# Kernel tuning notes

Hardware: AMD Instinct MI355X
Metric: run time of the kernel (lower is better)

The kernel has to match this reference:

```python
import jax, jax.numpy as jnp
import numpy as np

NUM_HEADS = 12


def setup_inputs() -> dict:
    key = jax.random.key(0)
    k1, k2, k3, k4, k5 = jax.random.split(key, 5)
    B, H, W, C = 8, 32, 32, 768
    x = jax.random.normal(k1, (B, H, W, C), dtype=jnp.float32)
    # torch nn.Linear weights: (out_features, in_features)
    qkv_w = jax.random.normal(k2, (3 * C, C), dtype=jnp.float32) * (C ** -0.5)
    qkv_b = jax.random.normal(k3, (3 * C,), dtype=jnp.float32) * 0.02
    proj_w = jax.random.normal(k4, (C, C), dtype=jnp.float32) * (C ** -0.5)
    proj_b = jax.random.normal(k5, (C,), dtype=jnp.float32) * 0.02
    return {"x": x, "qkv_w": qkv_w, "qkv_b": qkv_b, "proj_w": proj_w, "proj_b": proj_b}


def reference(x, qkv_w, qkv_b, proj_w, proj_b):
    B, H, W, C = x.shape
    nh = NUM_HEADS
    hd = C // nh
    scale = hd ** -0.5
    L = H * W
    # qkv projection: (B, L, 3C)
    qkv = jnp.einsum('bhwc,oc->bhwo', x, qkv_w) + qkv_b
    # -> (3, B*nh, L, hd)
    qkv = qkv.reshape(B, L, 3, nh, hd).transpose(2, 0, 3, 1, 4).reshape(3, B * nh, L, hd)
    q, k, v = qkv[0], qkv[1], qkv[2]
    # attention scores (B*nh, L, L)
    attn = jnp.einsum('bqd,bkd->bqk', q * scale, k)
    attn = jax.nn.softmax(attn, axis=-1)
    out = jnp.einsum('bqk,bkd->bqd', attn, v)  # (B*nh, L, hd)
    out = out.reshape(B, nh, H, W, hd).transpose(0, 2, 3, 1, 4).reshape(B, H, W, C)
    out = jnp.einsum('bhwc,oc->bhwo', out, proj_w) + proj_b
    return out
```

## Files before the change

kernel.cpp:

```cpp
#include <hip/hip_runtime.h>


typedef __attribute__((ext_vector_type(8))) __bf16 bf16x8;
typedef __attribute__((ext_vector_type(4))) __bf16 bf16x4;
typedef __attribute__((ext_vector_type(4))) float f32x4;

#define GLL16(g, l) __builtin_amdgcn_global_load_lds( \
    (const __attribute__((address_space(1))) void*)(g), \
    (__attribute__((address_space(3))) void*)(l), 16, 0, 0)

static __device__ __forceinline__ f32x4 mfma16(bf16x8 a, bf16x8 b, f32x4 c) {
  return __builtin_amdgcn_mfma_f32_16x16x32_bf16(a, b, c, 0, 0, 0);
}

static __device__ __forceinline__ float exp2_hw(float x) {
  return __builtin_amdgcn_exp2f(x);
}

static __device__ __forceinline__ int swz64(int row, int col) {
  return (row * 64 + col) ^ ((row & 7) << 3);
}

__global__ __launch_bounds__(256) void cvt_all(const float* __restrict__ x,
                                               const float* __restrict__ wq,
                                               const float* __restrict__ wp,
                                               __bf16* __restrict__ dst,
                                               int nx4, int nwq4, int total4) {
  const int i = blockIdx.x * 256 + threadIdx.x;
  if (i >= total4) return;
  const float* src;
  int off;
  if (i < nx4) { src = x; off = i; }
  else if (i < nx4 + nwq4) { src = wq; off = i - nx4; }
  else { src = wp; off = i - nx4 - nwq4; }
  const float4 v = *(const float4*)&src[(size_t)off * 4];
  bf16x4 o;
  o[0] = (__bf16)v.x; o[1] = (__bf16)v.y; o[2] = (__bf16)v.z; o[3] = (__bf16)v.w;
  *(bf16x4*)&dst[(size_t)i * 4] = o;
}

template <int EPI>
__global__ __launch_bounds__(256) void gemm_nt(const __bf16* __restrict__ A,
                                               const __bf16* __restrict__ Bw,
                                               const float* __restrict__ bias,
                                               float* __restrict__ out,
                                               __bf16* __restrict__ Qb,
                                               __bf16* __restrict__ Kb,
                                               __bf16* __restrict__ Vtb,
                                               int M, int N, int K) {
  __shared__ alignas(16) __bf16 smem[3 * 4096 * 2];
  const int tid = threadIdx.x;
  const int lane = tid & 63;
  const int wave = tid >> 6;
  const int wr = wave >> 1, wc = wave & 1;
  const int l15 = lane & 15, lhi = lane >> 4;
  const int mbase = blockIdx.x * 128;
  const int nbase = blockIdx.y * 128;

  f32x4 acc[4][4];
#pragma unroll
  for (int m = 0; m < 4; ++m)
#pragma unroll
    for (int n = 0; n < 4; ++n) acc[m][n] = (f32x4){0.f, 0.f, 0.f, 0.f};

  const int e0 = wave * 512 + lane * 8;
  const int e1 = e0 + 2048;
  const int ar0 = mbase + (e0 >> 5), ac0 = e0 & 31;
  const int ar1 = mbase + (e1 >> 5), ac1 = e1 & 31;
  const int br0 = nbase + (e0 >> 5);
  const int br1 = nbase + (e1 >> 5);

  const int nkt = K >> 5;

#define STAGE(t, bf) do { \
    const int kb_ = (t) << 5; \
    GLL16(A + (size_t)ar0 * K + kb_ + ac0, &smem[(bf) * 4096 + e0]); \
    GLL16(A + (size_t)ar1 * K + kb_ + ac1, &smem[(bf) * 4096 + e1]); \
    GLL16(Bw + (size_t)br0 * K + kb_ + ac0, &smem[12288 + (bf) * 4096 + e0]); \
    GLL16(Bw + (size_t)br1 * K + kb_ + ac1, &smem[12288 + (bf) * 4096 + e1]); \
  } while (0)

  STAGE(0, 0);
  STAGE(1, 1);

  int cur = 0, nx2 = 2;
  for (int kt = 0; kt < nkt; ++kt) {
    if (kt + 1 < nkt)
      asm volatile("s_waitcnt vmcnt(4)" ::: "memory");
    else
      asm volatile("s_waitcnt vmcnt(0)" ::: "memory");
    __builtin_amdgcn_s_barrier();
    asm volatile("" ::: "memory");
    if (kt + 2 < nkt) STAGE(kt + 2, nx2);

    const __bf16* bufA = &smem[cur * 4096];
    const __bf16* bufB = &smem[12288 + cur * 4096];
    bf16x8 a[4], b[4];
#pragma unroll
    for (int m = 0; m < 4; ++m)
      a[m] = *(const bf16x8*)&bufA[(wr * 64 + m * 16 + l15) * 32 + lhi * 8];
#pragma unroll
    for (int n = 0; n < 4; ++n)
      b[n] = *(const bf16x8*)&bufB[(wc * 64 + n * 16 + l15) * 32 + lhi * 8];
#pragma unroll
    for (int m = 0; m < 4; ++m)
#pragma unroll
      for (int n = 0; n < 4; ++n)
        acc[m][n] = mfma16(a[m], b[n], acc[m][n]);

    cur = (cur == 2) ? 0 : cur + 1;
    nx2 = (nx2 == 2) ? 0 : nx2 + 1;
  }
#undef STAGE

  if (EPI == 0 && nbase >= 1536) {
    __syncthreads();
    __bf16* ldsT = &smem[0];
#pragma unroll
    for (int n = 0; n < 4; ++n) {
      const int gl = wc * 64 + n * 16 + l15;
      const float bv = bias[nbase + gl];
#pragma unroll
      for (int m = 0; m < 4; ++m) {
        bf16x4 pk;
#pragma unroll
        for (int i = 0; i < 4; ++i) pk[i] = (__bf16)(acc[m][n][i] + bv);
        *(bf16x4*)&ldsT[gl * 136 + wr * 64 + m * 16 + lhi * 4] = pk;
      }
    }
    __syncthreads();
    const int r = tid >> 1;
    const int half = tid & 1;
    const int head = ((nbase - 1536) >> 6) + (r >> 6);
    const int d = r & 63;
    const int bb = mbase >> 10;
    const int lbase = mbase & 1023;
    __bf16* dst = Vtb + ((size_t)(bb * 12 + head) * 64 + d) * 1024 + lbase + half * 64;
    const __bf16* srcl = &ldsT[r * 136 + half * 64];
#pragma unroll
    for (int j = 0; j < 8; ++j)
      *(bf16x8*)&dst[j * 8] = *(const bf16x8*)&srcl[j * 8];
    return;
  }

#pragma unroll
  for (int n = 0; n < 4; ++n) {
    const int gcol = nbase + wc * 64 + n * 16 + l15;
    const float bv = bias[gcol];
    if (EPI == 1) {
#pragma unroll
      for (int m = 0; m < 4; ++m)
#pragma unroll
        for (int i = 0; i < 4; ++i) {
          const int grow = mbase + wr * 64 + m * 16 + lhi * 4 + i;
          out[(size_t)grow * N + gcol] = acc[m][n][i] + bv;
        }
    } else {
      const int three = gcol / 768;
      const int rem = gcol - three * 768;
      const int head = rem >> 6;
      const int d = rem & 63;
#pragma unroll
      for (int m = 0; m < 4; ++m)
#pragma unroll
        for (int i = 0; i < 4; ++i) {
          const int grow = mbase + wr * 64 + m * 16 + lhi * 4 + i;
          const int bb = grow >> 10;
          const int lrow = grow & 1023;
          const int bh = bb * 12 + head;
          const float v = acc[m][n][i] + bv;
          if (three == 0)
            Qb[((size_t)bh * 1024 + lrow) * 64 + d] = (__bf16)(v * 0.18033688f);
          else
            Kb[((size_t)bh * 1024 + lrow) * 64 + d] = (__bf16)v;
        }
    }
  }
}

__global__ __launch_bounds__(256) void attn_fwd(const __bf16* __restrict__ Q,
                                                const __bf16* __restrict__ Kg,
                                                const __bf16* __restrict__ Vt,
                                                __bf16* __restrict__ O) {
  __shared__ alignas(16) __bf16 lK[2][64 * 64];
  __shared__ alignas(16) __bf16 lV[2][64 * 64];
  __shared__ alignas(16) __bf16 lP[4][32 * 72];
  const int tid = threadIdx.x, lane = tid & 63, wave = tid >> 6;
  const int l15 = lane & 15, lhi = lane >> 4;
  const int bh = blockIdx.x, qt = blockIdx.y;
  const int b = bh / 12, head = bh % 12;

  bf16x8 q[2][2];
#pragma unroll
  for (int qn = 0; qn < 2; ++qn) {
    const int qrow = qt * 128 + wave * 32 + qn * 16 + l15;
#pragma unroll
    for (int kk = 0; kk < 2; ++kk)
      q[qn][kk] = *(const bf16x8*)&Q[((size_t)bh * 1024 + qrow) * 64 + kk * 32 + lhi * 8];
  }

  f32x4 o[2][4];
  float mrun[2], lrun[2];
#pragma unroll
  for (int m = 0; m < 2; ++m) {
#pragma unroll
    for (int n = 0; n < 4; ++n) o[m][n] = (f32x4){0.f, 0.f, 0.f, 0.f};
    mrun[m] = -3.0e38f; lrun[m] = 0.f;
  }

  const int q0b = wave * 1024 + lane * 16;
  const int q1b = q0b + 4096;
  const int p0b = q0b ^ (((q0b >> 7) & 7) << 4);
  const int p1b = q1b ^ (((q1b >> 7) & 7) << 4);
  const int e0 = q0b >> 1, e1 = q1b >> 1;
  const int kofs0 = p0b >> 1, kofs1 = p1b >> 1;
  const int vofs0 = (p0b >> 7) * 1024 + ((p0b & 127) >> 1);
  const int vofs1 = (p1b >> 7) * 1024 + ((p1b & 127) >> 1);

  const __bf16* kbase = Kg + (size_t)bh * 1024 * 64;
  const __bf16* vbase = Vt + (size_t)bh * 64 * 1024;

  GLL16(kbase + kofs0, &lK[0][e0]);
  GLL16(kbase + kofs1, &lK[0][e1]);
  GLL16(vbase + vofs0, &lV[0][e0]);
  GLL16(vbase + vofs1, &lV[0][e1]);
  __syncthreads();

  for (int kv = 0; kv < 16; ++kv) {
    const int cur = kv & 1;
    if (kv + 1 < 16) {
      const __bf16* knext = kbase + (kv + 1) * 4096;
      const int vadd = (kv + 1) * 64;
      GLL16(knext + kofs0, &lK[cur ^ 1][e0]);
      GLL16(knext + kofs1, &lK[cur ^ 1][e1]);
      GLL16(vbase + vadd + vofs0, &lV[cur ^ 1][e0]);
      GLL16(vbase + vadd + vofs1, &lV[cur ^ 1][e1]);
    }

    f32x4 s[4][2];
#pragma unroll
    for (int km = 0; km < 4; ++km) {
      bf16x8 k0 = *(const bf16x8*)&lK[cur][swz64(km * 16 + l15, lhi * 8)];
      bf16x8 k1 = *(const bf16x8*)&lK[cur][swz64(km * 16 + l15, 32 + lhi * 8)];
#pragma unroll
      for (int qn = 0; qn < 2; ++qn) {
        f32x4 z = (f32x4){0.f, 0.f, 0.f, 0.f};
        z = mfma16(k0, q[qn][0], z);
        z = mfma16(k1, q[qn][1], z);
        s[km][qn] = z;
      }
    }

    float lm[2];
#pragma unroll
    for (int qn = 0; qn < 2; ++qn) {
      float r = s[0][qn][0];
#pragma unroll
      for (int km = 0; km < 4; ++km)
#pragma unroll
        for (int i = 0; i < 4; ++i) r = fmaxf(r, s[km][qn][i]);
      lm[qn] = r;
    }

    const bool ok = (lm[0] - mrun[0] <= 8.f) && (lm[1] - mrun[1] <= 8.f);
    if (!__all(ok)) {
      float alpha[2];
#pragma unroll
      for (int qn = 0; qn < 2; ++qn) {
        float r = lm[qn];
        r = fmaxf(r, __shfl_xor(r, 16));
        r = fmaxf(r, __shfl_xor(r, 32));
        const float mnew = fmaxf(mrun[qn], r);
        alpha[qn] = exp2_hw(mrun[qn] - mnew);
        mrun[qn] = mnew;
        lrun[qn] *= alpha[qn];
      }
      float am[2][4];
#pragma unroll
      for (int m = 0; m < 2; ++m)
#pragma unroll
        for (int i = 0; i < 4; ++i) am[m][i] = __shfl(alpha[m], (lhi << 2) | i, 64);
#pragma unroll
      for (int m = 0; m < 2; ++m)
#pragma unroll
        for (int n = 0; n < 4; ++n)
#pragma unroll
          for (int i = 0; i < 4; ++i) o[m][n][i] *= am[m][i];
    }

#pragma unroll
    for (int qn = 0; qn < 2; ++qn) {
      float ps = 0.f;
#pragma unroll
      for (int km = 0; km < 4; ++km) {
        bf16x4 pk;
#pragma unroll
        for (int i = 0; i < 4; ++i) {
          const float p = exp2_hw(s[km][qn][i] - mrun[qn]);
          ps += p;
          pk[i] = (__bf16)p;
        }
        *(bf16x4*)&lP[wave][(qn * 16 + l15) * 72 + km * 16 + lhi * 4] = pk;
      }
      lrun[qn] += ps;
    }

    bf16x8 vf[4][2];
#pragma unroll
    for (int n = 0; n < 4; ++n)
#pragma unroll
      for (int kk = 0; kk < 2; ++kk)
        vf[n][kk] = *(const bf16x8*)&lV[cur][swz64(n * 16 + l15, kk * 32 + lhi * 8)];
#pragma unroll
    for (int m = 0; m < 2; ++m) {
      bf16x8 p0 = *(const bf16x8*)&lP[wave][(m * 16 + l15) * 72 + lhi * 8];
      bf16x8 p1 = *(const bf16x8*)&lP[wave][(m * 16 + l15) * 72 + 32 + lhi * 8];
#pragma unroll
      for (int n = 0; n < 4; ++n) {
        o[m][n] = mfma16(p0, vf[n][0], o[m][n]);
        o[m][n] = mfma16(p1, vf[n][1], o[m][n]);
      }
    }
    __syncthreads();
  }

  float inv2[2];
#pragma unroll
  for (int qn = 0; qn < 2; ++qn) {
    float r = lrun[qn];
    r += __shfl_xor(r, 16);
    r += __shfl_xor(r, 32);
    inv2[qn] = 1.f / r;
  }
  float im[2][4];
#pragma unroll
  for (int m = 0; m < 2; ++m)
#pragma unroll
    for (int i = 0; i < 4; ++i) im[m][i] = __shfl(inv2[m], (lhi << 2) | i, 64);
#pragma unroll
  for (int m = 0; m < 2; ++m)
#pragma unroll
    for (int i = 0; i < 4; ++i) {
      const int lrow = qt * 128 + wave * 32 + m * 16 + lhi * 4 + i;
#pragma unroll
      for (int n = 0; n < 4; ++n) {
        const int col = head * 64 + n * 16 + l15;
        O[((size_t)b * 1024 + lrow) * 768 + col] = (__bf16)(o[m][n][i] * im[m][i]);
      }
    }
}

extern "C" void kernel_launch(void* const* d_in, const int* in_sizes, int n_in,
                              void* d_out, int out_size, void* d_ws, size_t ws_size,
                              hipStream_t stream) {
  const float* x = (const float*)d_in[0];
  const float* qkv_w = (const float*)d_in[1];
  const float* qkv_b = (const float*)d_in[2];
  const float* proj_w = (const float*)d_in[3];
  const float* proj_b = (const float*)d_in[4];
  float* out = (float*)d_out;

  const size_t NX = (size_t)8192 * 768;
  const size_t NWQ = (size_t)2304 * 768;
  const size_t NWP = (size_t)768 * 768;
  const size_t SZ = (size_t)96 * 1024 * 64;

  __bf16* xb = (__bf16*)d_ws;
  __bf16* wqkvb = xb + NX;
  __bf16* wprojb = wqkvb + NWQ;
  __bf16* Q = wprojb + NWP;
  __bf16* K = Q + SZ;
  __bf16* Vt = K + SZ;
  __bf16* AO = Vt + SZ;

  const int nx4 = (int)(NX / 4), nwq4 = (int)(NWQ / 4), nwp4 = (int)(NWP / 4);
  const int total4 = nx4 + nwq4 + nwp4;
  cvt_all<<<(total4 + 255) / 256, 256, 0, stream>>>(x, qkv_w, proj_w, xb, nx4, nwq4, total4);

  gemm_nt<0><<<dim3(64, 18), 256, 0, stream>>>(xb, wqkvb, qkv_b, nullptr, Q, K, Vt,
                                               8192, 2304, 768);
  attn_fwd<<<dim3(96, 8), 256, 0, stream>>>(Q, K, Vt, AO);
  gemm_nt<1><<<dim3(64, 6), 256, 0, stream>>>(AO, wprojb, proj_b, out,
                                              nullptr, nullptr, nullptr, 8192, 768, 768);
}
```

Measured before the change: 123.5 us.

## Split attention block into 8 waves of 16 query rows each

The attention kernel now runs 512 threads (8 waves), each handling 16 query rows instead of 32. This halves per-wave register state and the K/V load work per thread, while K/V tiles in LDS are shared by twice as many waves. The goal is more waves in flight to hide latency. The cost is that each wave now reads the K and V fragments from LDS for only one 16-row MFMA tile instead of two, so LDS traffic per FLOP doubles, and barrier sync now spans 8 waves.

```diff
diff --git a/kernel.cpp b/kernel.cpp
--- a/kernel.cpp
+++ b/kernel.cpp
@@ -178,131 +178,99 @@
   }
 }
 
-__global__ __launch_bounds__(256) void attn_fwd(const __bf16* __restrict__ Q,
-                                                const __bf16* __restrict__ Kg,
-                                                const __bf16* __restrict__ Vt,
-                                                __bf16* __restrict__ O) {
+__global__ __launch_bounds__(512, 6) void attn_fwd(const __bf16* __restrict__ Q,
+                                                   const __bf16* __restrict__ Kg,
+                                                   const __bf16* __restrict__ Vt,
+                                                   __bf16* __restrict__ O) {
   __shared__ alignas(16) __bf16 lK[2][64 * 64];
   __shared__ alignas(16) __bf16 lV[2][64 * 64];
-  __shared__ alignas(16) __bf16 lP[4][32 * 72];
+  __shared__ alignas(16) __bf16 lP[8][16 * 72];
   const int tid = threadIdx.x, lane = tid & 63, wave = tid >> 6;
   const int l15 = lane & 15, lhi = lane >> 4;
   const int bh = blockIdx.x, qt = blockIdx.y;
   const int b = bh / 12, head = bh % 12;
 
-  bf16x8 q[2][2];
-#pragma unroll
-  for (int qn = 0; qn < 2; ++qn) {
-    const int qrow = qt * 128 + wave * 32 + qn * 16 + l15;
+  bf16x8 q[2];
+  {
+    const int qrow = qt * 128 + wave * 16 + l15;
 #pragma unroll
     for (int kk = 0; kk < 2; ++kk)
-      q[qn][kk] = *(const bf16x8*)&Q[((size_t)bh * 1024 + qrow) * 64 + kk * 32 + lhi * 8];
-  }
-
-  f32x4 o[2][4];
-  float mrun[2], lrun[2];
-#pragma unroll
-  for (int m = 0; m < 2; ++m) {
-#pragma unroll
-    for (int n = 0; n < 4; ++n) o[m][n] = (f32x4){0.f, 0.f, 0.f, 0.f};
-    mrun[m] = -3.0e38f; lrun[m] = 0.f;
-  }
-
-  const int q0b = wave * 1024 + lane * 16;
-  const int q1b = q0b + 4096;
+      q[kk] = *(const bf16x8*)&Q[((size_t)bh * 1024 + qrow) * 64 + kk * 32 + lhi * 8];
+  }
+
+  f32x4 o[4];
+  float mrun = -3.0e38f, lrun = 0.f;
+#pragma unroll
+  for (int n = 0; n < 4; ++n) o[n] = (f32x4){0.f, 0.f, 0.f, 0.f};
+
+  const int q0b = tid * 16;
   const int p0b = q0b ^ (((q0b >> 7) & 7) << 4);
-  const int p1b = q1b ^ (((q1b >> 7) & 7) << 4);
-  const int e0 = q0b >> 1, e1 = q1b >> 1;
-  const int kofs0 = p0b >> 1, kofs1 = p1b >> 1;
+  const int e0 = q0b >> 1;
+  const int kofs0 = p0b >> 1;
   const int vofs0 = (p0b >> 7) * 1024 + ((p0b & 127) >> 1);
-  const int vofs1 = (p1b >> 7) * 1024 + ((p1b & 127) >> 1);
 
   const __bf16* kbase = Kg + (size_t)bh * 1024 * 64;
   const __bf16* vbase = Vt + (size_t)bh * 64 * 1024;
 
   GLL16(kbase + kofs0, &lK[0][e0]);
-  GLL16(kbase + kofs1, &lK[0][e1]);
   GLL16(vbase + vofs0, &lV[0][e0]);
-  GLL16(vbase + vofs1, &lV[0][e1]);
   __syncthreads();
 
   for (int kv = 0; kv < 16; ++kv) {
     const int cur = kv & 1;
     if (kv + 1 < 16) {
-      const __bf16* knext = kbase + (kv + 1) * 4096;
-      const int vadd = (kv + 1) * 64;
-      GLL16(knext + kofs0, &lK[cur ^ 1][e0]);
-      GLL16(knext + kofs1, &lK[cur ^ 1][e1]);
-      GLL16(vbase + vadd + vofs0, &lV[cur ^ 1][e0]);
-      GLL16(vbase + vadd + vofs1, &lV[cur ^ 1][e1]);
-    }
-
-    f32x4 s[4][2];
+      GLL16(kbase + (kv + 1) * 4096 + kofs0, &lK[cur ^ 1][e0]);
+      GLL16(vbase + (kv + 1) * 64 + vofs0, &lV[cur ^ 1][e0]);
+    }
+
+    f32x4 s[4];
 #pragma unroll
     for (int km = 0; km < 4; ++km) {
       bf16x8 k0 = *(const bf16x8*)&lK[cur][swz64(km * 16 + l15, lhi * 8)];
       bf16x8 k1 = *(const bf16x8*)&lK[cur][swz64(km * 16 + l15, 32 + lhi * 8)];
-#pragma unroll
-      for (int qn = 0; qn < 2; ++qn) {
-        f32x4 z = (f32x4){0.f, 0.f, 0.f, 0.f};
-        z = mfma16(k0, q[qn][0], z);
-        z = mfma16(k1, q[qn][1], z);
-        s[km][qn] = z;
-      }
-    }
-
-    float lm[2];
-#pragma unroll
-    for (int qn = 0; qn < 2; ++qn) {
-      float r = s[0][qn][0];
-#pragma unroll
-      for (int km = 0; km < 4; ++km)
-#pragma unroll
-        for (int i = 0; i < 4; ++i) r = fmaxf(r, s[km][qn][i]);
-      lm[qn] = r;
-    }
-
-    const bool ok = (lm[0] - mrun[0] <= 8.f) && (lm[1] - mrun[1] <= 8.f);
-    if (!__all(ok)) {
-      float alpha[2];
-#pragma unroll
-      for (int qn = 0; qn < 2; ++qn) {
-        float r = lm[qn];
-        r = fmaxf(r, __shfl_xor(r, 16));
-        r = fmaxf(r, __shfl_xor(r, 32));
-        const float mnew = fmaxf(mrun[qn], r);
-        alpha[qn] = exp2_hw(mrun[qn] - mnew);
-        mrun[qn] = mnew;
-        lrun[qn] *= alpha[qn];
-      }
-      float am[2][4];
-#pragma unroll
-      for (int m = 0; m < 2; ++m)
-#pragma unroll
-        for (int i = 0; i < 4; ++i) am[m][i] = __shfl(alpha[m], (lhi << 2) | i, 64);
-#pragma unroll
-      for (int m = 0; m < 2; ++m)
-#pragma unroll
-        for (int n = 0; n < 4; ++n)
-#pragma unroll
-          for (int i = 0; i < 4; ++i) o[m][n][i] *= am[m][i];
-    }
-
-#pragma unroll
-    for (int qn = 0; qn < 2; ++qn) {
+      f32x4 z = (f32x4){0.f, 0.f, 0.f, 0.f};
+      z = mfma16(k0, q[0], z);
+      z = mfma16(k1, q[1], z);
+      s[km] = z;
+    }
+
+    float lm = s[0][0];
+#pragma unroll
+    for (int km = 0; km < 4; ++km)
+#pragma unroll
+      for (int i = 0; i < 4; ++i) lm = fmaxf(lm, s[km][i]);
+
+    if (!__all(lm - mrun <= 8.f)) {
+      float r = lm;
+      r = fmaxf(r, __shfl_xor(r, 16));
+      r = fmaxf(r, __shfl_xor(r, 32));
+      const float mnew = fmaxf(mrun, r);
+      const float alpha = exp2_hw(mrun - mnew);
+      mrun = mnew;
+      lrun *= alpha;
+      float am[4];
+#pragma unroll
+      for (int i = 0; i < 4; ++i) am[i] = __shfl(alpha, (lhi << 2) | i, 64);
+#pragma unroll
+      for (int n = 0; n < 4; ++n)
+#pragma unroll
+        for (int i = 0; i < 4; ++i) o[n][i] *= am[i];
+    }
+
+    {
       float ps = 0.f;
 #pragma unroll
       for (int km = 0; km < 4; ++km) {
         bf16x4 pk;
 #pragma unroll
         for (int i = 0; i < 4; ++i) {
-          const float p = exp2_hw(s[km][qn][i] - mrun[qn]);
+          const float p = exp2_hw(s[km][i] - mrun);
           ps += p;
           pk[i] = (__bf16)p;
         }
-        *(bf16x4*)&lP[wave][(qn * 16 + l15) * 72 + km * 16 + lhi * 4] = pk;
+        *(bf16x4*)&lP[wave][l15 * 72 + km * 16 + lhi * 4] = pk;
       }
-      lrun[qn] += ps;
+      lrun += ps;
     }
 
     bf16x8 vf[4][2];
@@ -311,43 +279,34 @@
 #pragma unroll
       for (int kk = 0; kk < 2; ++kk)
         vf[n][kk] = *(const bf16x8*)&lV[cur][swz64(n * 16 + l15, kk * 32 + lhi * 8)];
-#pragma unroll
-    for (int m = 0; m < 2; ++m) {
-      bf16x8 p0 = *(const bf16x8*)&lP[wave][(m * 16 + l15) * 72 + lhi * 8];
-      bf16x8 p1 = *(const bf16x8*)&lP[wave][(m * 16 + l15) * 72 + 32 + lhi * 8];
+    {
+      bf16x8 p0 = *(const bf16x8*)&lP[wave][l15 * 72 + lhi * 8];
+      bf16x8 p1 = *(const bf16x8*)&lP[wave][l15 * 72 + 32 + lhi * 8];
 #pragma unroll
       for (int n = 0; n < 4; ++n) {
-        o[m][n] = mfma16(p0, vf[n][0], o[m][n]);
-        o[m][n] = mfma16(p1, vf[n][1], o[m][n]);
+        o[n] = mfma16(p0, vf[n][0], o[n]);
+        o[n] = mfma16(p1, vf[n][1], o[n]);
       }
     }
     __syncthreads();
   }
 
-  float inv2[2];
-#pragma unroll
-  for (int qn = 0; qn < 2; ++qn) {
-    float r = lrun[qn];
-    r += __shfl_xor(r, 16);
-    r += __shfl_xor(r, 32);
-    inv2[qn] = 1.f / r;
-  }
-  float im[2][4];
-#pragma unroll
-  for (int m = 0; m < 2; ++m)
-#pragma unroll
-    for (int i = 0; i < 4; ++i) im[m][i] = __shfl(inv2[m], (lhi << 2) | i, 64);
-#pragma unroll
-  for (int m = 0; m < 2; ++m)
-#pragma unroll
-    for (int i = 0; i < 4; ++i) {
-      const int lrow = qt * 128 + wave * 32 + m * 16 + lhi * 4 + i;
-#pragma unroll
-      for (int n = 0; n < 4; ++n) {
-        const int col = head * 64 + n * 16 + l15;
-        O[((size_t)b * 1024 + lrow) * 768 + col] = (__bf16)(o[m][n][i] * im[m][i]);
-      }
-    }
+  float r = lrun;
+  r += __shfl_xor(r, 16);
+  r += __shfl_xor(r, 32);
+  const float inv = 1.f / r;
+  float im[4];
+#pragma unroll
+  for (int i = 0; i < 4; ++i) im[i] = __shfl(inv, (lhi << 2) | i, 64);
+#pragma unroll
+  for (int i = 0; i < 4; ++i) {
+    const int lrow = qt * 128 + wave * 16 + lhi * 4 + i;
+#pragma unroll
+    for (int n = 0; n < 4; ++n) {
+      const int col = head * 64 + n * 16 + l15;
+      O[((size_t)b * 1024 + lrow) * 768 + col] = (__bf16)(o[n][i] * im[i]);
+    }
+  }
 }
 
 extern "C" void kernel_launch(void* const* d_in, const int* in_sizes, int n_in,
@@ -379,7 +338,7 @@
 
   gemm_nt<0><<<dim3(64, 18), 256, 0, stream>>>(xb, wqkvb, qkv_b, nullptr, Q, K, Vt,
                                                8192, 2304, 768);
-  attn_fwd<<<dim3(96, 8), 256, 0, stream>>>(Q, K, Vt, AO);
+  attn_fwd<<<dim3(96, 8), 512, 0, stream>>>(Q, K, Vt, AO);
   gemm_nt<1><<<dim3(64, 6), 256, 0, stream>>>(AO, wprojb, proj_b, out,
                                               nullptr, nullptr, nullptr, 8192, 768, 768);
 }
```

New measurement: 116.1 us. 6.0% less time.
